# Kernel optimization log

Measured on AMD Instinct MI355X. Metric: run time of the kernel, lower is better.

Reference implementation:

```python
import jax, jax.numpy as jnp
import numpy as np

DIM = 768
NUM_HEADS = 12
HEAD_DIM = DIM // NUM_HEADS
SCALE = HEAD_DIM ** -0.5
NEG = -9e15


def setup_inputs() -> dict:
    key = jax.random.key(0)
    ks = jax.random.split(key, 8)
    B, N, M, C = 4, 1024, 2048, DIM
    q = jax.random.normal(ks[0], (B, N, C), dtype=jnp.float32)
    kv = jax.random.normal(ks[1], (B, M, C), dtype=jnp.float32)
    mask = jax.random.randint(ks[2], (B, 1, N, M), 0, 2, dtype=jnp.int32)
    s = 1.0 / np.sqrt(C)
    Wq = jax.random.normal(ks[3], (C, C), dtype=jnp.float32) * s      # nn.Linear(dim, dim), no bias
    Wkv = jax.random.normal(ks[4], (2 * C, C), dtype=jnp.float32) * s  # nn.Linear(dim, 2*dim), no bias
    Wproj = jax.random.normal(ks[5], (C, C), dtype=jnp.float32) * s
    bproj = jax.random.normal(ks[6], (C,), dtype=jnp.float32) * s
    return {"q": q, "kv": kv, "Wq": Wq, "Wkv": Wkv, "Wproj": Wproj, "bproj": bproj, "mask": mask}


def reference(q, kv, Wq, Wkv, Wproj, bproj, mask):
    B, M, C = kv.shape
    _, N, _ = q.shape
    H, d = NUM_HEADS, HEAD_DIM
    # kv projection -> [B, M, 2, H, d] -> k, v: [B, H, M, d]
    kvp = (kv @ Wkv.T).reshape(B, M, 2, H, d)
    k = kvp[:, :, 0].transpose(0, 2, 1, 3)
    v = kvp[:, :, 1].transpose(0, 2, 1, 3)
    # q projection -> [B, H, N, d], pre-scaled
    qp = (q @ Wq.T).reshape(B, N, H, d).transpose(0, 2, 1, 3) * SCALE
    attn = jnp.einsum('bhnd,bhmd->bhnm', qp, k)  # [B, H, N, M]
    attn = jnp.where(mask == 0, NEG, attn)
    attn = jax.nn.softmax(attn, axis=-1)
    # attn_drop / proj_drop have rate 0.0 (eval): identity
    x = jnp.einsum('bhnm,bhmd->bhnd', attn, v)
    x = x.transpose(0, 2, 1, 3).reshape(B, N, C)
    x = x @ Wproj.T + bproj
    return x
```

## Files before the change

### kernel.cpp

```cpp
#include <hip/hip_runtime.h>
#include <hip/hip_bf16.h>


typedef short    s16x8  __attribute__((ext_vector_type(8)));
typedef short    s16x4  __attribute__((ext_vector_type(4)));
typedef float    f32x4  __attribute__((ext_vector_type(4)));
typedef _Float16 f16x8  __attribute__((ext_vector_type(8)));
typedef _Float16 f16x4  __attribute__((ext_vector_type(4)));
typedef _Float16 f16x2  __attribute__((ext_vector_type(2)));

#define NUM_H 12
#define DIM   768
#define NQ    1024
#define MK    2048
#define QK_SCALE_LOG2E 0.18033688f

__device__ __forceinline__ short f2h(float v) {
    _Float16 h = (_Float16)v;
    return __builtin_bit_cast(short, h);
}
__device__ __forceinline__ f32x4 mfma16x32(f16x8 a, f16x8 b, f32x4 c) {
    return __builtin_amdgcn_mfma_f32_16x16x32_f16(a, b, c, 0, 0, 0);
}
__device__ __forceinline__ f16x2 pk2h(float a, float b) {
    return __builtin_bit_cast(f16x2, __builtin_amdgcn_cvt_pkrtz(a, b));
}

__global__ __launch_bounds__(256) void prep_kernel(
    const float* __restrict__ q, const float* __restrict__ kv,
    const float* __restrict__ Wq, const float* __restrict__ Wkv,
    const float* __restrict__ Wp, const int* __restrict__ mask,
    short* __restrict__ q_h, short* __restrict__ kv_h,
    short* __restrict__ Wq_h, short* __restrict__ Wkv_h,
    short* __restrict__ Wp_h, unsigned char* __restrict__ mbytes)
{
    int bid = blockIdx.x;
    if (bid < 5760) {
        const float* s; short* d; long base;
        if (bid < 1536)      { s = q;   d = q_h;   base = (long)bid * 2048; }
        else if (bid < 4608) { s = kv;  d = kv_h;  base = (long)(bid - 1536) * 2048; }
        else if (bid < 4896) { s = Wq;  d = Wq_h;  base = (long)(bid - 4608) * 2048; }
        else if (bid < 5472) { s = Wkv; d = Wkv_h; base = (long)(bid - 4896) * 2048; }
        else                 { s = Wp;  d = Wp_h;  base = (long)(bid - 5472) * 2048; }
        long i = base + threadIdx.x * 8;
        float4 a = *(const float4*)(s + i);
        float4 b = *(const float4*)(s + i + 4);
        s16x8 r;
        r[0] = f2h(a.x); r[1] = f2h(a.y); r[2] = f2h(a.z); r[3] = f2h(a.w);
        r[4] = f2h(b.x); r[5] = f2h(b.y); r[6] = f2h(b.z); r[7] = f2h(b.w);
        *(s16x8*)(d + i) = r;
    } else {
        long base = (long)(bid - 5760) * 2048 + threadIdx.x * 8;
        int4 m0 = *(const int4*)(mask + base);
        int4 m1 = *(const int4*)(mask + base + 4);
        unsigned v = (unsigned)(m0.x != 0)        | ((unsigned)(m0.y != 0) << 1)
                   | ((unsigned)(m0.z != 0) << 2) | ((unsigned)(m0.w != 0) << 3)
                   | ((unsigned)(m1.x != 0) << 4) | ((unsigned)(m1.y != 0) << 5)
                   | ((unsigned)(m1.z != 0) << 6) | ((unsigned)(m1.w != 0) << 7);
        mbytes[base >> 3] = (unsigned char)v;
    }
}

__device__ __forceinline__ void gemm_core(
    short* smem,
    const short* __restrict__ A, const short* __restrict__ Bt,
    int Ncols, int mode, const float* __restrict__ bias,
    short* __restrict__ outb, short* __restrict__ outb2,
    float* __restrict__ outf, int bid)
{
    short (*As)[72] = (short(*)[72])smem;
    short (*Bs)[72] = (short(*)[72])(smem + 9216);

    int ntiles = Ncols >> 7;
    int m0 = (bid / ntiles) << 7;
    int n0 = (bid % ntiles) << 7;
    int t = threadIdx.x;
    int w = t >> 6, lane = t & 63, quad = lane >> 4, l16 = lane & 15;
    int wm = (w & 1) << 6, wn = (w >> 1) << 6;

    f32x4 zero4 = {0.f, 0.f, 0.f, 0.f};
    f32x4 acc[4][4];
    for (int i = 0; i < 4; i++)
        for (int j = 0; j < 4; j++) acc[i][j] = zero4;

    int lr = t >> 1;
    int lc = (t & 1) << 5;
    const short* Ap = A + (long)(m0 + lr) * DIM + lc;
    const short* Bp = Bt + (long)(n0 + lr) * DIM + lc;

    s16x8 a0[4], b0[4], a1[4], b1[4];
    #pragma unroll
    for (int c = 0; c < 4; c++) {
        a0[c] = *(const s16x8*)(Ap + c * 8);
        b0[c] = *(const s16x8*)(Bp + c * 8);
        a1[c] = *(const s16x8*)(Ap + 64 + c * 8);
        b1[c] = *(const s16x8*)(Bp + 64 + c * 8);
    }

    auto mfma_tile = [&]() {
        #pragma unroll
        for (int kh = 0; kh < 2; kh++) {
            f16x8 af[4], bfr[4];
            #pragma unroll
            for (int i = 0; i < 4; i++)
                af[i] = __builtin_bit_cast(f16x8,
                    *(const s16x8*)&As[wm + i * 16 + l16][kh * 32 + quad * 8]);
            #pragma unroll
            for (int j = 0; j < 4; j++)
                bfr[j] = __builtin_bit_cast(f16x8,
                    *(const s16x8*)&Bs[wn + j * 16 + l16][kh * 32 + quad * 8]);
            #pragma unroll
            for (int i = 0; i < 4; i++)
                #pragma unroll
                for (int j = 0; j < 4; j++)
                    acc[i][j] = mfma16x32(af[i], bfr[j], acc[i][j]);
        }
    };

    for (int kt = 0; kt < DIM; kt += 128) {
        __syncthreads();
        #pragma unroll
        for (int c = 0; c < 4; c++) {
            *(s16x8*)&As[lr][lc + c * 8] = a0[c];
            *(s16x8*)&Bs[lr][lc + c * 8] = b0[c];
        }
        __syncthreads();
        if (kt + 128 < DIM) {
            #pragma unroll
            for (int c = 0; c < 4; c++) {
                a0[c] = *(const s16x8*)(Ap + kt + 128 + c * 8);
                b0[c] = *(const s16x8*)(Bp + kt + 128 + c * 8);
            }
        }
        mfma_tile();
        __syncthreads();
        #pragma unroll
        for (int c = 0; c < 4; c++) {
            *(s16x8*)&As[lr][lc + c * 8] = a1[c];
            *(s16x8*)&Bs[lr][lc + c * 8] = b1[c];
        }
        __syncthreads();
        if (kt + 192 < DIM) {
            #pragma unroll
            for (int c = 0; c < 4; c++) {
                a1[c] = *(const s16x8*)(Ap + kt + 192 + c * 8);
                b1[c] = *(const s16x8*)(Bp + kt + 192 + c * 8);
            }
        }
        mfma_tile();
    }

    __syncthreads();

    if (mode == 2) {
        #pragma unroll
        for (int i = 0; i < 4; i++)
            #pragma unroll
            for (int j = 0; j < 4; j++)
                #pragma unroll
                for (int r = 0; r < 4; r++) {
                    int row = m0 + wm + i * 16 + quad * 4 + r;
                    int col = n0 + wn + j * 16 + l16;
                    outf[(long)row * DIM + col] = acc[i][j][r] + bias[col];
                }
        return;
    }

    short (*Cs)[136] = (short(*)[136])smem;
    bool vreg = (mode == 1) && (n0 >= DIM);

    if (!vreg) {
        float sc = (mode == 0) ? QK_SCALE_LOG2E : 1.0f;
        #pragma unroll
        for (int i = 0; i < 4; i++)
            #pragma unroll
            for (int j = 0; j < 4; j++)
                #pragma unroll
                for (int r = 0; r < 4; r++)
                    Cs[wm + i * 16 + quad * 4 + r][wn + j * 16 + l16] =
                        f2h(acc[i][j][r] * sc);
    } else {
        #pragma unroll
        for (int i = 0; i < 4; i++)
            #pragma unroll
            for (int j = 0; j < 4; j++) {
                int c = wn + j * 16 + l16;
                int r0 = wm + i * 16 + quad * 4;
                s16x4 pk;
                pk[0] = f2h(acc[i][j][0]); pk[1] = f2h(acc[i][j][1]);
                pk[2] = f2h(acc[i][j][2]); pk[3] = f2h(acc[i][j][3]);
                *(s16x4*)&Cs[c][r0] = pk;
            }
    }
    __syncthreads();

    if (!vreg) {
        int hb2 = n0 >> 6;
        long rowsN = (mode == 0) ? NQ : MK;
        int b = (int)(m0 / rowsN);
        int rb = (int)(m0 % rowsN);
        short* ob0 = outb + ((long)(b * NUM_H + hb2) * rowsN + rb) * 64;
        short* ob1 = outb + ((long)(b * NUM_H + hb2 + 1) * rowsN + rb) * 64;
        #pragma unroll
        for (int k2 = 0; k2 < 8; k2++) {
            int ch = k2 * 256 + t;
            int half = ch >> 10, off = ch & 1023;
            s16x8 vd = *(const s16x8*)&Cs[off >> 3][(half << 6) + ((off & 7) << 3)];
            *(s16x8*)((half ? ob1 : ob0) + off * 8) = vd;
        }
    } else {
        int hb2 = (n0 - DIM) >> 6;
        int b = m0 >> 11, rb = m0 & 2047;
        #pragma unroll
        for (int k2 = 0; k2 < 8; k2++) {
            int ch = k2 * 256 + t;
            int c = ch >> 4, woff = (ch & 15) << 3;
            s16x8 vd = *(const s16x8*)&Cs[c][woff];
            int half = c >> 6, dd = c & 63;
            *(s16x8*)(outb2 + (((long)(b * NUM_H + hb2 + half) * 64 + dd) * MK + rb) + woff) = vd;
        }
    }
}

__global__ __launch_bounds__(256) void gemm12_kernel(
    const short* __restrict__ qh, const short* __restrict__ Wqh,
    const short* __restrict__ kvh, const short* __restrict__ Wkvh,
    short* __restrict__ qp, short* __restrict__ kk, short* __restrict__ vt)
{
    __shared__ short smem[18432];
    if (blockIdx.x < 192)
        gemm_core(smem, qh, Wqh, 768, 0, nullptr, qp, nullptr, nullptr, blockIdx.x);
    else
        gemm_core(smem, kvh, Wkvh, 1536, 1, nullptr, kk, vt, nullptr, blockIdx.x - 192);
}

__global__ __launch_bounds__(256) void gemm3_kernel(
    const short* __restrict__ xb, const short* __restrict__ Wph,
    const float* __restrict__ bias, float* __restrict__ out)
{
    __shared__ short smem[18432];
    gemm_core(smem, xb, Wph, 768, 2, bias, nullptr, nullptr, out, blockIdx.x);
}

__global__ __launch_bounds__(256) void attn_kernel(
    const short* __restrict__ qp, const short* __restrict__ kk,
    const short* __restrict__ vt, const unsigned* __restrict__ mb,
    short* __restrict__ xb)
{
    __shared__ short qs[64][72];
    __shared__ short ks[64][72];
    __shared__ short vs[64][72];

    int bid = blockIdx.x;
    int bh = bid % 48;
    int nt = bid / 48;
    int h = bh % NUM_H, b = bh / NUM_H;
    int n0 = nt << 6;
    int t = threadIdx.x, w = t >> 6, lane = t & 63, quad = lane >> 4, l16 = lane & 15;

    const short* qbase = qp + ((long)bh * NQ + n0) * 64;
    const short* kbase = kk + (long)bh * MK * 64;
    const short* vbase = vt + (long)bh * 64 * MK;
    const unsigned* mrow = mb + ((long)b * NQ + n0 + (w << 4) + l16) * 64;

    {
        int qr = t >> 2, c0 = (t & 3) << 4;
        *(s16x8*)&qs[qr][c0]     = *(const s16x8*)(qbase + qr * 64 + c0);
        *(s16x8*)&qs[qr][c0 + 8] = *(const s16x8*)(qbase + qr * 64 + c0 + 8);
    }
    __syncthreads();
    f16x8 bq[2];
    #pragma unroll
    for (int kh = 0; kh < 2; kh++)
        bq[kh] = __builtin_bit_cast(f16x8,
            *(const s16x8*)&qs[(w << 4) + l16][kh * 32 + quad * 8]);

    int sr = t >> 2, c0 = (t & 3) << 4;
    int pr = (sr & 32) + ((sr & 4) << 2) + ((sr & 24) >> 1) + (sr & 3);
    const short* kp = kbase + (long)sr * 64 + c0;
    const short* vp = vbase + (long)sr * MK + c0;

    s16x8 k0 = *(const s16x8*)(kp);
    s16x8 k1 = *(const s16x8*)(kp + 8);
    s16x8 v0 = *(const s16x8*)(vp);
    s16x8 v1 = *(const s16x8*)(vp + 8);
    uint2 mwv = *(const uint2*)(mrow);

    f32x4 zero4 = {0.f, 0.f, 0.f, 0.f};
    f32x4 o[4], ol = zero4;
    for (int j = 0; j < 4; j++) o[j] = zero4;
    const f16x8 ones = {(_Float16)1.f, (_Float16)1.f, (_Float16)1.f, (_Float16)1.f,
                        (_Float16)1.f, (_Float16)1.f, (_Float16)1.f, (_Float16)1.f};

    for (int mt = 0; mt < MK; mt += 64) {
        __syncthreads();
        *(s16x8*)&ks[pr][c0]     = k0;
        *(s16x8*)&ks[pr][c0 + 8] = k1;
        *(s16x8*)&vs[sr][c0]     = v0;
        *(s16x8*)&vs[sr][c0 + 8] = v1;
        unsigned cm0 = mwv.x, cm1 = mwv.y;
        __syncthreads();
        if (mt + 64 < MK) {
            k0 = *(const s16x8*)(kp + (long)(mt + 64) * 64);
            k1 = *(const s16x8*)(kp + (long)(mt + 64) * 64 + 8);
            v0 = *(const s16x8*)(vp + mt + 64);
            v1 = *(const s16x8*)(vp + mt + 64 + 8);
            mwv = *(const uint2*)(mrow + ((mt + 64) >> 5));
        }

        f32x4 s[4];
        #pragma unroll
        for (int jj = 0; jj < 4; jj++) s[jj] = zero4;
        #pragma unroll
        for (int kh = 0; kh < 2; kh++)
            #pragma unroll
            for (int jj = 0; jj < 4; jj++) {
                f16x8 ak = __builtin_bit_cast(f16x8,
                    *(const s16x8*)&ks[jj * 16 + l16][kh * 32 + quad * 8]);
                s[jj] = mfma16x32(ak, bq[kh], s[jj]);
            }

        f16x8 pa[2];
        #pragma unroll
        for (int j2 = 0; j2 < 2; j2++) {
            unsigned wsel = j2 ? cm1 : cm0;
            f16x2 pk[4];
            #pragma unroll
            for (int sub = 0; sub < 2; sub++) {
                unsigned bits = wsel >> ((quad << 3) + (sub << 2));
                const f32x4& sv = s[j2 * 2 + sub];
                float p0 = (bits & 1u)        ? __builtin_amdgcn_exp2f(sv[0]) : 0.f;
                float p1 = ((bits >> 1) & 1u) ? __builtin_amdgcn_exp2f(sv[1]) : 0.f;
                float p2 = ((bits >> 2) & 1u) ? __builtin_amdgcn_exp2f(sv[2]) : 0.f;
                float p3 = ((bits >> 3) & 1u) ? __builtin_amdgcn_exp2f(sv[3]) : 0.f;
                pk[sub * 2]     = pk2h(p0, p1);
                pk[sub * 2 + 1] = pk2h(p2, p3);
            }
            f16x4 lo = __builtin_shufflevector(pk[0], pk[1], 0, 1, 2, 3);
            f16x4 hi = __builtin_shufflevector(pk[2], pk[3], 0, 1, 2, 3);
            pa[j2] = __builtin_shufflevector(lo, hi, 0, 1, 2, 3, 4, 5, 6, 7);
        }

        #pragma unroll
        for (int j2 = 0; j2 < 2; j2++) {
            ol = mfma16x32(pa[j2], ones, ol);
            #pragma unroll
            for (int jd = 0; jd < 4; jd++) {
                f16x8 bv = __builtin_bit_cast(f16x8,
                    *(const s16x8*)&vs[jd * 16 + l16][j2 * 32 + quad * 8]);
                o[jd] = mfma16x32(pa[j2], bv, o[jd]);
            }
        }
    }

    float linv[4];
    #pragma unroll
    for (int rr = 0; rr < 4; rr++) linv[rr] = 1.0f / ol[rr];
    short (*ps)[72] = (short(*)[72])&qs[w << 4];
    #pragma unroll
    for (int jd = 0; jd < 4; jd++)
        #pragma unroll
        for (int rr = 0; rr < 4; rr++)
            ps[quad * 4 + rr][jd * 16 + l16] = f2h(o[jd][rr] * linv[rr]);

    #pragma unroll
    for (int k2 = 0; k2 < 2; k2++) {
        int row = (lane >> 3) + k2 * 8;
        int cc = (lane & 7) << 3;
        s16x8 vd = *(const s16x8*)&ps[row][cc];
        *(s16x8*)(xb + ((long)b * NQ + n0 + (w << 4) + row) * DIM + h * 64 + cc) = vd;
    }
}

extern "C" void kernel_launch(void* const* d_in, const int* in_sizes, int n_in,
                              void* d_out, int out_size, void* d_ws, size_t ws_size,
                              hipStream_t stream)
{
    const float* q     = (const float*)d_in[0];
    const float* kv    = (const float*)d_in[1];
    const float* Wq    = (const float*)d_in[2];
    const float* Wkv   = (const float*)d_in[3];
    const float* Wproj = (const float*)d_in[4];
    const float* bproj = (const float*)d_in[5];
    const int*   mask  = (const int*)d_in[6];
    float* out = (float*)d_out;

    char* ws = (char*)d_ws;
    short* q_h   = (short*)ws; ws += (size_t)4096 * 768 * 2;
    short* kv_h  = (short*)ws; ws += (size_t)8192 * 768 * 2;
    short* Wq_h  = (short*)ws; ws += (size_t)768 * 768 * 2;
    short* Wkv_h = (short*)ws; ws += (size_t)1536 * 768 * 2;
    short* Wp_h  = (short*)ws; ws += (size_t)768 * 768 * 2;
    short* qp    = (short*)ws; ws += (size_t)4096 * 768 * 2;
    short* kk    = (short*)ws; ws += (size_t)8192 * 768 * 2;
    short* vt    = (short*)ws; ws += (size_t)8192 * 768 * 2;
    short* xb    = (short*)ws; ws += (size_t)4096 * 768 * 2;
    unsigned char* mbytes = (unsigned char*)ws;

    prep_kernel<<<9856, 256, 0, stream>>>(q, kv, Wq, Wkv, Wproj, mask,
                                          q_h, kv_h, Wq_h, Wkv_h, Wp_h, mbytes);
    gemm12_kernel<<<960, 256, 0, stream>>>(q_h, Wq_h, kv_h, Wkv_h, qp, kk, vt);
    attn_kernel<<<768, 256, 0, stream>>>(qp, kk, vt, (const unsigned*)mbytes, xb);
    gemm3_kernel<<<192, 256, 0, stream>>>(xb, Wp_h, bproj, out);
}
```

Measured before the change: 214.4 us.

## Process 128 query rows per attention block to reuse K/V tiles

Each attention block now covers 128 query rows instead of 64, and each wave handles two 16-row sub-tiles, so every K/V tile staged in LDS feeds twice as many MFMAs. This halves global K/V traffic and per-tile sync overhead relative to compute. In exchange the grid drops from 768 to 384 blocks, which is below a couple of waves over the MI355X's 256 CUs, and per-thread register use roughly doubles for the accumulators. Both of these can hurt occupancy and latency hiding.

```diff
diff --git a/kernel.cpp b/kernel.cpp
--- a/kernel.cpp
+++ b/kernel.cpp
@@ -247,7 +247,7 @@
     const short* __restrict__ vt, const unsigned* __restrict__ mb,
     short* __restrict__ xb)
 {
-    __shared__ short qs[64][72];
+    __shared__ short qs[128][72];
     __shared__ short ks[64][72];
     __shared__ short vs[64][72];
 
@@ -255,25 +255,29 @@
     int bh = bid % 48;
     int nt = bid / 48;
     int h = bh % NUM_H, b = bh / NUM_H;
-    int n0 = nt << 6;
+    int n0 = nt << 7;
     int t = threadIdx.x, w = t >> 6, lane = t & 63, quad = lane >> 4, l16 = lane & 15;
 
     const short* qbase = qp + ((long)bh * NQ + n0) * 64;
     const short* kbase = kk + (long)bh * MK * 64;
     const short* vbase = vt + (long)bh * 64 * MK;
-    const unsigned* mrow = mb + ((long)b * NQ + n0 + (w << 4) + l16) * 64;
+    const unsigned* mrow0 = mb + ((long)b * NQ + n0 + (w << 5) + l16) * 64;
+    const unsigned* mrow1 = mrow0 + 16 * 64;
 
     {
-        int qr = t >> 2, c0 = (t & 3) << 4;
-        *(s16x8*)&qs[qr][c0]     = *(const s16x8*)(qbase + qr * 64 + c0);
-        *(s16x8*)&qs[qr][c0 + 8] = *(const s16x8*)(qbase + qr * 64 + c0 + 8);
+        int qr = t >> 1, c0 = (t & 1) << 5;
+        #pragma unroll
+        for (int c = 0; c < 4; c++)
+            *(s16x8*)&qs[qr][c0 + c * 8] = *(const s16x8*)(qbase + qr * 64 + c0 + c * 8);
     }
     __syncthreads();
-    f16x8 bq[2];
+    f16x8 bq[2][2];
     #pragma unroll
-    for (int kh = 0; kh < 2; kh++)
-        bq[kh] = __builtin_bit_cast(f16x8,
-            *(const s16x8*)&qs[(w << 4) + l16][kh * 32 + quad * 8]);
+    for (int s2 = 0; s2 < 2; s2++)
+        #pragma unroll
+        for (int kh = 0; kh < 2; kh++)
+            bq[s2][kh] = __builtin_bit_cast(f16x8,
+                *(const s16x8*)&qs[(w << 5) + (s2 << 4) + l16][kh * 32 + quad * 8]);
 
     int sr = t >> 2, c0 = (t & 3) << 4;
     int pr = (sr & 32) + ((sr & 4) << 2) + ((sr & 24) >> 1) + (sr & 3);
@@ -284,11 +288,16 @@
     s16x8 k1 = *(const s16x8*)(kp + 8);
     s16x8 v0 = *(const s16x8*)(vp);
     s16x8 v1 = *(const s16x8*)(vp + 8);
-    uint2 mwv = *(const uint2*)(mrow);
+    uint2 mwv0 = *(const uint2*)(mrow0);
+    uint2 mwv1 = *(const uint2*)(mrow1);
 
     f32x4 zero4 = {0.f, 0.f, 0.f, 0.f};
-    f32x4 o[4], ol = zero4;
-    for (int j = 0; j < 4; j++) o[j] = zero4;
+    f32x4 o[2][4], ol[2];
+    #pragma unroll
+    for (int s2 = 0; s2 < 2; s2++) {
+        ol[s2] = zero4;
+        for (int j = 0; j < 4; j++) o[s2][j] = zero4;
+    }
     const f16x8 ones = {(_Float16)1.f, (_Float16)1.f, (_Float16)1.f, (_Float16)1.f,
                         (_Float16)1.f, (_Float16)1.f, (_Float16)1.f, (_Float16)1.f};
 
@@ -298,77 +307,86 @@
         *(s16x8*)&ks[pr][c0 + 8] = k1;
         *(s16x8*)&vs[sr][c0]     = v0;
         *(s16x8*)&vs[sr][c0 + 8] = v1;
-        unsigned cm0 = mwv.x, cm1 = mwv.y;
+        unsigned cm[2][2] = {{mwv0.x, mwv0.y}, {mwv1.x, mwv1.y}};
         __syncthreads();
         if (mt + 64 < MK) {
             k0 = *(const s16x8*)(kp + (long)(mt + 64) * 64);
             k1 = *(const s16x8*)(kp + (long)(mt + 64) * 64 + 8);
             v0 = *(const s16x8*)(vp + mt + 64);
             v1 = *(const s16x8*)(vp + mt + 64 + 8);
-            mwv = *(const uint2*)(mrow + ((mt + 64) >> 5));
-        }
-
-        f32x4 s[4];
-        #pragma unroll
-        for (int jj = 0; jj < 4; jj++) s[jj] = zero4;
+            mwv0 = *(const uint2*)(mrow0 + ((mt + 64) >> 5));
+            mwv1 = *(const uint2*)(mrow1 + ((mt + 64) >> 5));
+        }
+
+        f32x4 s[2][4];
+        #pragma unroll
+        for (int jj = 0; jj < 4; jj++) { s[0][jj] = zero4; s[1][jj] = zero4; }
         #pragma unroll
         for (int kh = 0; kh < 2; kh++)
             #pragma unroll
             for (int jj = 0; jj < 4; jj++) {
                 f16x8 ak = __builtin_bit_cast(f16x8,
                     *(const s16x8*)&ks[jj * 16 + l16][kh * 32 + quad * 8]);
-                s[jj] = mfma16x32(ak, bq[kh], s[jj]);
-            }
-
-        f16x8 pa[2];
+                s[0][jj] = mfma16x32(ak, bq[0][kh], s[0][jj]);
+                s[1][jj] = mfma16x32(ak, bq[1][kh], s[1][jj]);
+            }
+
+        f16x8 pa[2][2];
+        #pragma unroll
+        for (int s2 = 0; s2 < 2; s2++)
+            #pragma unroll
+            for (int j2 = 0; j2 < 2; j2++) {
+                unsigned wsel = cm[s2][j2];
+                f16x2 pk[4];
+                #pragma unroll
+                for (int sub = 0; sub < 2; sub++) {
+                    unsigned bits = wsel >> ((quad << 3) + (sub << 2));
+                    const f32x4& sv = s[s2][j2 * 2 + sub];
+                    float p0 = (bits & 1u)        ? __builtin_amdgcn_exp2f(sv[0]) : 0.f;
+                    float p1 = ((bits >> 1) & 1u) ? __builtin_amdgcn_exp2f(sv[1]) : 0.f;
+                    float p2 = ((bits >> 2) & 1u) ? __builtin_amdgcn_exp2f(sv[2]) : 0.f;
+                    float p3 = ((bits >> 3) & 1u) ? __builtin_amdgcn_exp2f(sv[3]) : 0.f;
+                    pk[sub * 2]     = pk2h(p0, p1);
+                    pk[sub * 2 + 1] = pk2h(p2, p3);
+                }
+                f16x4 lo = __builtin_shufflevector(pk[0], pk[1], 0, 1, 2, 3);
+                f16x4 hi = __builtin_shufflevector(pk[2], pk[3], 0, 1, 2, 3);
+                pa[s2][j2] = __builtin_shufflevector(lo, hi, 0, 1, 2, 3, 4, 5, 6, 7);
+            }
+
         #pragma unroll
         for (int j2 = 0; j2 < 2; j2++) {
-            unsigned wsel = j2 ? cm1 : cm0;
-            f16x2 pk[4];
-            #pragma unroll
-            for (int sub = 0; sub < 2; sub++) {
-                unsigned bits = wsel >> ((quad << 3) + (sub << 2));
-                const f32x4& sv = s[j2 * 2 + sub];
-                float p0 = (bits & 1u)        ? __builtin_amdgcn_exp2f(sv[0]) : 0.f;
-                float p1 = ((bits >> 1) & 1u) ? __builtin_amdgcn_exp2f(sv[1]) : 0.f;
-                float p2 = ((bits >> 2) & 1u) ? __builtin_amdgcn_exp2f(sv[2]) : 0.f;
-                float p3 = ((bits >> 3) & 1u) ? __builtin_amdgcn_exp2f(sv[3]) : 0.f;
-                pk[sub * 2]     = pk2h(p0, p1);
-                pk[sub * 2 + 1] = pk2h(p2, p3);
-            }
-            f16x4 lo = __builtin_shufflevector(pk[0], pk[1], 0, 1, 2, 3);
-            f16x4 hi = __builtin_shufflevector(pk[2], pk[3], 0, 1, 2, 3);
-            pa[j2] = __builtin_shufflevector(lo, hi, 0, 1, 2, 3, 4, 5, 6, 7);
-        }
-
-        #pragma unroll
-        for (int j2 = 0; j2 < 2; j2++) {
-            ol = mfma16x32(pa[j2], ones, ol);
+            ol[0] = mfma16x32(pa[0][j2], ones, ol[0]);
+            ol[1] = mfma16x32(pa[1][j2], ones, ol[1]);
             #pragma unroll
             for (int jd = 0; jd < 4; jd++) {
                 f16x8 bv = __builtin_bit_cast(f16x8,
                     *(const s16x8*)&vs[jd * 16 + l16][j2 * 32 + quad * 8]);
-                o[jd] = mfma16x32(pa[j2], bv, o[jd]);
-            }
-        }
-    }
-
-    float linv[4];
+                o[0][jd] = mfma16x32(pa[0][j2], bv, o[0][jd]);
+                o[1][jd] = mfma16x32(pa[1][j2], bv, o[1][jd]);
+            }
+        }
+    }
+
+    __syncthreads();
     #pragma unroll
-    for (int rr = 0; rr < 4; rr++) linv[rr] = 1.0f / ol[rr];
-    short (*ps)[72] = (short(*)[72])&qs[w << 4];
+    for (int s2 = 0; s2 < 2; s2++) {
+        float linv[4];
+        #pragma unroll
+        for (int rr = 0; rr < 4; rr++) linv[rr] = 1.0f / ol[s2][rr];
+        #pragma unroll
+        for (int jd = 0; jd < 4; jd++)
+            #pragma unroll
+            for (int rr = 0; rr < 4; rr++)
+                qs[(w << 5) + (s2 << 4) + quad * 4 + rr][jd * 16 + l16] =
+                    f2h(o[s2][jd][rr] * linv[rr]);
+    }
     #pragma unroll
-    for (int jd = 0; jd < 4; jd++)
-        #pragma unroll
-        for (int rr = 0; rr < 4; rr++)
-            ps[quad * 4 + rr][jd * 16 + l16] = f2h(o[jd][rr] * linv[rr]);
-
-    #pragma unroll
-    for (int k2 = 0; k2 < 2; k2++) {
-        int row = (lane >> 3) + k2 * 8;
+    for (int k2 = 0; k2 < 4; k2++) {
+        int row = (w << 5) + (lane >> 3) + k2 * 8;
         int cc = (lane & 7) << 3;
-        s16x8 vd = *(const s16x8*)&ps[row][cc];
-        *(s16x8*)(xb + ((long)b * NQ + n0 + (w << 4) + row) * DIM + h * 64 + cc) = vd;
+        s16x8 vd = *(const s16x8*)&qs[row][cc];
+        *(s16x8*)(xb + ((long)b * NQ + n0 + row) * DIM + h * 64 + cc) = vd;
     }
 }
 
@@ -400,6 +418,6 @@
     prep_kernel<<<9856, 256, 0, stream>>>(q, kv, Wq, Wkv, Wproj, mask,
                                           q_h, kv_h, Wq_h, Wkv_h, Wp_h, mbytes);
     gemm12_kernel<<<960, 256, 0, stream>>>(q_h, Wq_h, kv_h, Wkv_h, qp, kk, vt);
-    attn_kernel<<<768, 256, 0, stream>>>(qp, kk, vt, (const unsigned*)mbytes, xb);
+    attn_kernel<<<384, 256, 0, stream>>>(qp, kk, vt, (const unsigned*)mbytes, xb);
     gemm3_kernel<<<192, 256, 0, stream>>>(xb, Wp_h, bproj, out);
 }
```

Result: slower. 223.0 us (+4.0%).
